# Kernel optimization log

Measured on AMD Instinct MI355X. Metric: run time of the kernel, lower is better.

The kernel has to match this reference:

```python
import jax, jax.numpy as jnp
import numpy as np

B, N, C, H = 2, 2048, 256, 8
HD = C // H
LN_EPS = 1e-5
BN_EPS = 1e-5  # eval-mode BatchNorm with running_mean=0, running_var=1


def _ln(x, g, b):
    # LayerNorm over last dim
    m = jnp.mean(x, axis=-1, keepdims=True)
    v = jnp.mean((x - m) ** 2, axis=-1, keepdims=True)
    return (x - m) * jax.lax.rsqrt(v + LN_EPS) * g + b


def _ln_cn(x, g, b):
    # x: [B,C,N], normalize over C (torch does transpose -> LN -> transpose)
    return jnp.swapaxes(_ln(jnp.swapaxes(x, 1, 2), g, b), 1, 2)


def _cdist(a, b):
    # a: [B,N,D], b: [B,M,D] -> [B,N,M] euclidean
    d2 = (jnp.sum(a * a, -1)[:, :, None] + jnp.sum(b * b, -1)[:, None, :]
          - 2.0 * jnp.einsum('bnd,bmd->bnm', a, b))
    return jnp.sqrt(jnp.maximum(d2, 0.0))


def _conv1x1(w, x, b=None):
    # w: [O,C], x: [B,C,N]
    y = jnp.einsum('oc,bcn->bon', w, x)
    return y if b is None else y + b[None, :, None]


def setup_inputs() -> dict:
    key = jax.random.key(0)
    ks = jax.random.split(key, 32)
    s = 0.02
    inp = {
        'xyz_A': jax.random.normal(ks[0], (B, N, 3), jnp.float32),
        'featA': jax.random.normal(ks[1], (B, C, N), jnp.float32),
        'xyz_B': jax.random.normal(ks[2], (B, N, 3), jnp.float32),
        'featB': jax.random.normal(ks[3], (B, C, N), jnp.float32),
        'ln_in_g': jnp.ones((C,), jnp.float32),
        'ln_in_b': jnp.zeros((C,), jnp.float32),
        'Wq': jax.random.normal(ks[4], (C, C), jnp.float32) * s,
        'bq': jnp.zeros((C,), jnp.float32),
        'Wk': jax.random.normal(ks[5], (C, C), jnp.float32) * s,
        'bk': jnp.zeros((C,), jnp.float32),
        'Wv': jax.random.normal(ks[6], (C, C), jnp.float32) * s,
        'bv': jnp.zeros((C,), jnp.float32),
        'sb_w1': jax.random.normal(ks[7], (H // 2, 1), jnp.float32) * s,
        'sb_bn_g': jnp.ones((H // 2,), jnp.float32),
        'sb_bn_b': jnp.zeros((H // 2,), jnp.float32),
        'sb_w2': jax.random.normal(ks[8], (H, H // 2), jnp.float32) * s,
        'sb_b2': jnp.zeros((H,), jnp.float32),
        'Wqd': jax.random.normal(ks[9], (C, C), jnp.float32) * s,
        'bqd': jnp.zeros((C,), jnp.float32),
        'Wkd': jax.random.normal(ks[10], (C, C), jnp.float32) * s,
        'bkd': jnp.zeros((C,), jnp.float32),
        'ln_sim_g': jnp.ones((C,), jnp.float32),
        'ln_sim_b': jnp.zeros((C,), jnp.float32),
        'ln_dis_g': jnp.ones((C,), jnp.float32),
        'ln_dis_b': jnp.zeros((C,), jnp.float32),
        'Wf1': jax.random.normal(ks[11], (2 * C, 3 * C), jnp.float32) * s,
        'bnf_g': jnp.ones((2 * C,), jnp.float32),
        'bnf_b': jnp.zeros((2 * C,), jnp.float32),
        'Wf2': jax.random.normal(ks[12], (C, 2 * C), jnp.float32) * s,
        'bf2': jnp.zeros((C,), jnp.float32),
    }
    return inp


def reference(xyz_A, featA, xyz_B, featB, ln_in_g, ln_in_b, Wq, bq, Wk, bk, Wv, bv,
              sb_w1, sb_bn_g, sb_bn_b, sb_w2, sb_b2, Wqd, bqd, Wkd, bkd,
              ln_sim_g, ln_sim_b, ln_dis_g, ln_dis_b, Wf1, bnf_g, bnf_b, Wf2, bf2):
    featA_norm = _ln_cn(featA, ln_in_g, ln_in_b)  # [B,C,N]

    # spatial bias: cdist -> 1x1 conv2d MLP over channel dim
    dist = _cdist(xyz_A, xyz_B)  # [B,N,N]
    h = jnp.einsum('oi,binm->bonm', sb_w1, -dist[:, None])  # [B,H/2,N,N]
    h = h * (sb_bn_g / np.sqrt(1.0 + BN_EPS))[None, :, None, None] + sb_bn_b[None, :, None, None]
    h = jax.nn.relu(h)
    spatial_bias = jnp.einsum('oi,binm->bonm', sb_w2, h) + sb_b2[None, :, None, None]  # [B,H,N,N]

    # similarity path
    q = _conv1x1(Wq, featA_norm, bq).reshape(B, H, HD, N).transpose(0, 1, 3, 2)  # [B,H,N,hd]
    k = _conv1x1(Wk, featB, bk).reshape(B, H, HD, N).transpose(0, 1, 3, 2)
    sim_scores = jnp.einsum('bhnd,bhmd->bhnm', q, k) / np.sqrt(HD) + spatial_bias

    # dissimilarity path: feature-space cdist
    qd = jnp.swapaxes(_conv1x1(Wqd, featA_norm, bqd), 1, 2)  # [B,N,C]
    kd = jnp.swapaxes(_conv1x1(Wkd, featB, bkd), 1, 2)
    dissim_scores = _cdist(qd, kd)[:, None] + spatial_bias  # [B,H,N,N]

    sim_w = jax.nn.softmax(sim_scores, axis=-1)
    dis_w = jax.nn.softmax(dissim_scores, axis=-1)

    v = _conv1x1(Wv, featB, bv).reshape(B, H, HD, N).transpose(0, 1, 3, 2)  # [B,H,N,hd]
    ctx_sim = jnp.einsum('bhnm,bhmd->bhnd', sim_w, v).transpose(0, 1, 3, 2).reshape(B, C, N)
    ctx_sim = _ln_cn(ctx_sim, ln_sim_g, ln_sim_b)
    ctx_dis = jnp.einsum('bhnm,bhmd->bhnd', dis_w, v).transpose(0, 1, 3, 2).reshape(B, C, N)
    ctx_dis = _ln_cn(ctx_dis, ln_dis_g, ln_dis_b)

    fused_in = jnp.concatenate([featA_norm, ctx_sim, ctx_dis], axis=1)  # [B,3C,N]
    f = jnp.einsum('oc,bcn->bon', Wf1, fused_in)
    f = f * (bnf_g / np.sqrt(1.0 + BN_EPS))[None, :, None] + bnf_b[None, :, None]
    f = jax.nn.relu(f)
    fused = jnp.einsum('oc,bcn->bon', Wf2, f) + bf2[None, :, None]

    return fused + featA  # residual (in_channel == out_channel -> Identity)
```

## Files before the change

kernel.cpp:

```cpp
#include <hip/hip_runtime.h>
#include <math.h>

#define B_ 2
#define N_ 2048
#define C_ 256
#define H_ 8
#define HD_ 32
constexpr float LN_EPS_ = 1e-5f;
constexpr float BN_EPS_ = 1e-5f;
constexpr float LOG2E_ = 1.4426950408889634f;
constexpr float ISDL_ = 0.17677669529663687f * 1.4426950408889634f;

typedef __attribute__((ext_vector_type(8))) short bf16x8;
typedef __attribute__((ext_vector_type(4))) float f32x4;

static __device__ inline ushort f2bf(float x) {
    union { float f; uint u; } c{x};
    uint r = (c.u + 0x7FFF + ((c.u >> 16) & 1)) >> 16;
    return (ushort)r;
}
static __device__ inline float bf2f(ushort u) {
    union { uint i; float f; } c; c.i = ((uint)u) << 16; return c.f;
}
static __device__ inline float lane_bcast(float v, int srclane) {
    return __int_as_float(__builtin_amdgcn_ds_bpermute(srclane * 4, __float_as_int(v)));
}
static __device__ inline uint pack_bf2(float lo, float hi) {
    uint ul = __float_as_uint(lo) + 0x8000u;
    uint uh = __float_as_uint(hi) + 0x8000u;
    return __builtin_amdgcn_perm(uh, ul, 0x07060302u);
}

__global__ __launch_bounds__(256)
void k_wconv(const float* __restrict__ Wq, const float* __restrict__ Wqd,
             const float* __restrict__ Wk, const float* __restrict__ Wkd,
             const float* __restrict__ Wv, const float* __restrict__ Wf1,
             const float* __restrict__ Wf2, ushort* __restrict__ dst)
{
    size_t e0 = ((size_t)blockIdx.x * 256 + threadIdx.x) * 8;
    const float* src = Wq; size_t base = 0;
    if (e0 >= 65536)  { src = Wqd; base = 65536; }
    if (e0 >= 131072) { src = Wk;  base = 131072; }
    if (e0 >= 196608) { src = Wkd; base = 196608; }
    if (e0 >= 262144) { src = Wv;  base = 262144; }
    if (e0 >= 327680) { src = Wf1; base = 327680; }
    if (e0 >= 720896) { src = Wf2; base = 720896; }
    float4 a = *(const float4*)(src + (e0 - base));
    float4 b = *(const float4*)(src + (e0 - base) + 4);
    ushort o[8] = {f2bf(a.x), f2bf(a.y), f2bf(a.z), f2bf(a.w),
                   f2bf(b.x), f2bf(b.y), f2bf(b.z), f2bf(b.w)};
    *(uint4*)(dst + e0) = *(uint4*)o;
}

__global__ __launch_bounds__(512)
void k_bconcat(const float* __restrict__ bq, const float* __restrict__ bqd,
               const float* __restrict__ bk, const float* __restrict__ bkd,
               float* __restrict__ bqqd, float* __restrict__ bkkd)
{
    int t = threadIdx.x;
    bqqd[t] = (t < 256) ? bq[t] : bqd[t - 256];
    bkkd[t] = (t < 256) ? bk[t] : bkd[t - 256];
}

template<bool DO_LN>
__global__ __launch_bounds__(256)
void k_ln_transpose(const float* __restrict__ x,
                    const float* __restrict__ g,
                    const float* __restrict__ bt,
                    ushort* __restrict__ out, int ld)
{
    __shared__ float tile[C_][65];
    __shared__ float red_s[4][64];
    __shared__ float red_q[4][64];
    __shared__ float ms[64];
    __shared__ float rs[64];

    const int b  = blockIdx.x / (N_ / 64);
    const int n0 = (blockIdx.x % (N_ / 64)) * 64;
    const int tid = threadIdx.x;

    for (int i = 0; i < 64; ++i) {
        int c = i * 4 + (tid >> 6);
        int n = tid & 63;
        tile[c][n] = x[((size_t)b * C_ + c) * N_ + n0 + n];
    }
    __syncthreads();

    float gv = 0.f, bv = 0.f;
    if (DO_LN) { gv = g[tid]; bv = bt[tid]; }

    if (DO_LN) {
        const int nl = tid & 63, part = tid >> 6;
        float s = 0.f, q = 0.f;
        for (int j = 0; j < 64; ++j) {
            float v = tile[part * 64 + j][nl];
            s += v; q += v * v;
        }
        red_s[part][nl] = s; red_q[part][nl] = q;
        __syncthreads();
        if (tid < 64) {
            float ss = red_s[0][tid] + red_s[1][tid] + red_s[2][tid] + red_s[3][tid];
            float qq = red_q[0][tid] + red_q[1][tid] + red_q[2][tid] + red_q[3][tid];
            float mean = ss * (1.0f / C_);
            float var  = qq * (1.0f / C_) - mean * mean;
            ms[tid] = mean;
            rs[tid] = rsqrtf(var + LN_EPS_);
        }
        __syncthreads();
    }

    for (int i = 0; i < 64; ++i) {
        float v = tile[tid][i];
        if (DO_LN) v = (v - ms[i]) * rs[i] * gv + bv;
        out[((size_t)b * N_ + n0 + i) * ld + tid] = f2bf(v);
    }
}

template<int EPI, int OUT>
__global__ __launch_bounds__(256)
void k_gemm_bf(const ushort* __restrict__ A, int lda, size_t sAz,
               const ushort* __restrict__ Bw, int ldb, size_t sBz,
               void* __restrict__ Cout_, int ldc, size_t sCz,
               int K,
               const float* __restrict__ aux1,
               const float* __restrict__ aux2)
{
    const int z = blockIdx.z;
    A  += (size_t)z * sAz;
    Bw += (size_t)z * sBz;

    const int r0 = blockIdx.x * 64;
    const int c0 = blockIdx.y * 64;
    const int tid = threadIdx.x;
    const int w = tid >> 6, lane = tid & 63;
    const int wr = w >> 1, wc = w & 1;
    const int ql = lane & 15, g = lane >> 4;

    __shared__ ushort As[64][40];
    __shared__ ushort Bs[64][40];

    f32x4 acc[2][2] = {};
    const int srow = tid >> 2;
    const int sk   = (tid & 3) * 8;

    for (int k0 = 0; k0 < K; k0 += 32) {
        bf16x8 av = *(const bf16x8*)&A[(size_t)(r0 + srow) * lda + k0 + sk];
        bf16x8 bv = *(const bf16x8*)&Bw[(size_t)(c0 + srow) * ldb + k0 + sk];
        __syncthreads();
        *(bf16x8*)&As[srow][sk] = av;
        *(bf16x8*)&Bs[srow][sk] = bv;
        __syncthreads();
        bf16x8 af[2], bf[2];
        #pragma unroll
        for (int i = 0; i < 2; ++i) {
            af[i] = *(const bf16x8*)&As[wr * 32 + i * 16 + ql][8 * g];
            bf[i] = *(const bf16x8*)&Bs[wc * 32 + i * 16 + ql][8 * g];
        }
        #pragma unroll
        for (int mi = 0; mi < 2; ++mi)
            #pragma unroll
            for (int ni = 0; ni < 2; ++ni)
                acc[mi][ni] = __builtin_amdgcn_mfma_f32_16x16x32_bf16(af[mi], bf[ni], acc[mi][ni], 0, 0, 0);
    }

    const float inv_bn = rsqrtf(1.0f + BN_EPS_);
    float*  Cf = (float*)Cout_  + (size_t)z * sCz;
    ushort* Cb = (ushort*)Cout_ + (size_t)z * sCz;
    #pragma unroll
    for (int mi = 0; mi < 2; ++mi) {
        #pragma unroll
        for (int ni = 0; ni < 2; ++ni) {
            #pragma unroll
            for (int r = 0; r < 4; ++r) {
                int row = r0 + wr * 32 + mi * 16 + 4 * g + r;
                int col = c0 + wc * 32 + ni * 16 + ql;
                float v = acc[mi][ni][r];
                if (EPI == 0) {
                    v += aux1[col];
                } else if (EPI == 1) {
                    float qnv = aux1[(size_t)z * N_ + row];
                    float knv = aux2[(size_t)z * N_ + col];
                    v = sqrtf(fmaxf(qnv + knv - 2.0f * v, 0.f)) * LOG2E_;
                } else if (EPI == 2) {
                    v = fmaxf(v * (aux1[col] * inv_bn) + aux2[col], 0.f);
                } else if (EPI == 3) {
                    v += aux1[row];
                }
                if (OUT == 0) Cf[(size_t)row * ldc + col] = v;
                else          Cb[(size_t)row * ldc + col] = f2bf(v);
            }
        }
    }
}

__global__ __launch_bounds__(256)
void k_rownorm(const ushort* __restrict__ x, int ld, float* __restrict__ outn)
{
    const int r = blockIdx.x * 4 + (threadIdx.x >> 6);
    const int lane = threadIdx.x & 63;
    uint2 pv = *(const uint2*)&x[(size_t)r * ld + lane * 4];
    float v0 = bf2f((ushort)(pv.x & 0xffff)), v1 = bf2f((ushort)(pv.x >> 16));
    float v2 = bf2f((ushort)(pv.y & 0xffff)), v3 = bf2f((ushort)(pv.y >> 16));
    float s = v0 * v0 + v1 * v1 + v2 * v2 + v3 * v3;
    #pragma unroll
    for (int off = 32; off; off >>= 1) s += __shfl_xor(s, off);
    if (lane == 0) outn[r] = s;
}

#define QLD_ 512
__global__ __launch_bounds__(512, 4)
void k_attn6(const ushort* __restrict__ q_bf,
             const ushort* __restrict__ k_bf,
             const ushort* __restrict__ v_c,
             const float* __restrict__ xyzA,
             const float* __restrict__ xyzB,
             const ushort* __restrict__ cdb,
             const float* __restrict__ sb_w1, const float* __restrict__ sb_bn_g,
             const float* __restrict__ sb_bn_b, const float* __restrict__ sb_w2,
             const float* __restrict__ sb_b2,
             ushort* __restrict__ pc,
             float* __restrict__ pml)
{
    __shared__ float  biasL[4][16][66];
    __shared__ float  cds[16][68];
    __shared__ ushort ps[8][16][72];
    __shared__ float  w2Ls[4][4];
    __shared__ float  b2Ls[4];

    const int n0 = blockIdx.x * 16;
    const int b  = blockIdx.y;
    const int hg   = blockIdx.z & 1;
    const int half = blockIdx.z >> 1;
    const size_t bN = (size_t)b * N_;
    const int tid = threadIdx.x;
    const int w = tid >> 6, lane = tid & 63;
    const int path = w >> 2, hl = w & 3;
    const int h = hg * 4 + hl;
    const int ql = lane & 15, g = lane >> 4;

    if (tid < 4) {
        b2Ls[tid] = sb_b2[hg * 4 + tid] * LOG2E_;
        #pragma unroll
        for (int i = 0; i < 4; ++i) w2Ls[tid][i] = sb_w2[(hg * 4 + tid) * 4 + i] * LOG2E_;
    }

    const float inv_bn = rsqrtf(1.0f + BN_EPS_);
    float w1s_[4], bnb_[4];
    #pragma unroll
    for (int i = 0; i < 4; ++i) {
        w1s_[i] = sb_w1[i] * sb_bn_g[i] * inv_bn;
        bnb_[i] = sb_bn_b[i];
    }

    const int cq = tid >> 5, cm2 = tid & 31;
    const float ax = xyzA[(bN + n0 + cq) * 3 + 0];
    const float ay = xyzA[(bN + n0 + cq) * 3 + 1];
    const float az = xyzA[(bN + n0 + cq) * 3 + 2];

    bf16x8 qfrag = {};
    if (path == 0)
        qfrag = *(const bf16x8*)&q_bf[(bN + n0 + ql) * QLD_ + h * 32 + 8 * g];

    float m_i = -INFINITY, l_i = 0.f;
    f32x4 ctx0 = {0.f, 0.f, 0.f, 0.f};
    f32x4 ctx1 = {0.f, 0.f, 0.f, 0.f};
    const f32x4 zf = {0.f, 0.f, 0.f, 0.f};

    const int tBeg = half * (N_ / 128);
    const int tEnd = tBeg + (N_ / 128);

    for (int t = tBeg; t < tEnd; ++t) {
        const int m0 = t * 64;
        __syncthreads();

        {
            const int mA = m0 + 2 * cm2;
            const float* pb = xyzB + (bN + mA) * 3;
            float bx0 = pb[0], by0 = pb[1], bz0 = pb[2];
            float bx1 = pb[3], by1 = pb[4], bz1 = pb[5];
            float dx0 = ax - bx0, dy0 = ay - by0, dz0 = az - bz0;
            float dx1 = ax - bx1, dy1 = ay - by1, dz1 = az - bz1;
            float d0 = sqrtf(dx0 * dx0 + dy0 * dy0 + dz0 * dz0);
            float d1 = sqrtf(dx1 * dx1 + dy1 * dy1 + dz1 * dz1);
            float f0[4], f1[4];
            #pragma unroll
            for (int i = 0; i < 4; ++i) {
                f0[i] = fmaxf(fmaf(-w1s_[i], d0, bnb_[i]), 0.f);
                f1[i] = fmaxf(fmaf(-w1s_[i], d1, bnb_[i]), 0.f);
            }
            #pragma unroll
            for (int hh = 0; hh < 4; ++hh) {
                const f32x4 w2v = *(const f32x4*)w2Ls[hh];
                float b0 = b2Ls[hh], b1 = b2Ls[hh];
                #pragma unroll
                for (int i = 0; i < 4; ++i) {
                    b0 = fmaf(w2v[i], f0[i], b0);
                    b1 = fmaf(w2v[i], f1[i], b1);
                }
                *(float2*)&biasL[hh][cq][2 * cm2] = make_float2(b0, b1);
            }
            uint cv = *(const uint*)&cdb[(bN + n0 + cq) * (size_t)N_ + mA];
            cds[cq][2 * cm2]     = __uint_as_float(cv << 16);
            cds[cq][2 * cm2 + 1] = __uint_as_float(cv & 0xffff0000u);
        }
        __syncthreads();

        bf16x8 af[4];
        if (path == 0) {
            #pragma unroll
            for (int mt = 0; mt < 4; ++mt)
                af[mt] = *(const bf16x8*)&k_bf[(bN + m0 + mt * 16 + ql) * QLD_ + h * 32 + 8 * g];
        }
        bf16x8 vb[2][2];
        #pragma unroll
        for (int kb = 0; kb < 2; ++kb)
            #pragma unroll
            for (int dt = 0; dt < 2; ++dt)
                vb[kb][dt] = *(const bf16x8*)&v_c[((size_t)b * C_ + h * 32 + dt * 16 + ql) * N_ + m0 + kb * 32 + 8 * g];

        float s[16];
        #pragma unroll
        for (int mt = 0; mt < 4; ++mt) {
            float2 blo = *(const float2*)&biasL[hl][ql][16 * mt + 4 * g];
            float2 bhi = *(const float2*)&biasL[hl][ql][16 * mt + 4 * g + 2];
            s[4 * mt + 0] = blo.x;
            s[4 * mt + 1] = blo.y;
            s[4 * mt + 2] = bhi.x;
            s[4 * mt + 3] = bhi.y;
        }

        if (path == 0) {
            #pragma unroll
            for (int mt = 0; mt < 4; ++mt) {
                f32x4 sf = __builtin_amdgcn_mfma_f32_16x16x32_bf16(af[mt], qfrag, zf, 0, 0, 0);
                #pragma unroll
                for (int r = 0; r < 4; ++r)
                    s[4 * mt + r] = fmaf(sf[r], ISDL_, s[4 * mt + r]);
            }
        } else {
            #pragma unroll
            for (int mt = 0; mt < 4; ++mt) {
                f32x4 cv = *(const f32x4*)&cds[ql][16 * mt + 4 * g];
                #pragma unroll
                for (int r = 0; r < 4; ++r)
                    s[4 * mt + r] += cv[r];
            }
        }

        float t0 = fmaxf(s[0], s[1]),   t1 = fmaxf(s[2], s[3]);
        float t2 = fmaxf(s[4], s[5]),   t3 = fmaxf(s[6], s[7]);
        float t4 = fmaxf(s[8], s[9]),   t5 = fmaxf(s[10], s[11]);
        float t6 = fmaxf(s[12], s[13]), t7 = fmaxf(s[14], s[15]);
        t0 = fmaxf(t0, t1); t2 = fmaxf(t2, t3);
        t4 = fmaxf(t4, t5); t6 = fmaxf(t6, t7);
        float tmax = fmaxf(fmaxf(t0, t2), fmaxf(t4, t6));
        tmax = fmaxf(tmax, __shfl_xor(tmax, 16));
        tmax = fmaxf(tmax, __shfl_xor(tmax, 32));
        if (!__all(tmax <= m_i + 8.0f)) {
            float mnew = fmaxf(m_i, tmax);
            float scl = exp2f(m_i - mnew);
            l_i *= scl;
            #pragma unroll
            for (int r = 0; r < 4; ++r) {
                float sr = lane_bcast(scl, 4 * g + r);
                ctx0[r] *= sr; ctx1[r] *= sr;
            }
            m_i = mnew;
        }
        float lsum = 0.f;
        #pragma unroll
        for (int j = 0; j < 16; ++j) {
            float pj = exp2f(s[j] - m_i);
            s[j] = pj;
            lsum += pj;
        }
        lsum += __shfl_xor(lsum, 16);
        lsum += __shfl_xor(lsum, 32);
        l_i += lsum;

        #pragma unroll
        for (int mt = 0; mt < 4; ++mt) {
            uint2 pk;
            pk.x = pack_bf2(s[4 * mt + 0], s[4 * mt + 1]);
            pk.y = pack_bf2(s[4 * mt + 2], s[4 * mt + 3]);
            *(uint2*)&ps[w][ql][16 * mt + 4 * g] = pk;
        }

        #pragma unroll
        for (int kb = 0; kb < 2; ++kb) {
            bf16x8 pa = *(const bf16x8*)&ps[w][ql][kb * 32 + 8 * g];
            ctx0 = __builtin_amdgcn_mfma_f32_16x16x32_bf16(pa, vb[kb][0], ctx0, 0, 0, 0);
            ctx1 = __builtin_amdgcn_mfma_f32_16x16x32_bf16(pa, vb[kb][1], ctx1, 0, 0, 0);
        }
    }

    const size_t sl = (size_t)(half * 2 + path) * (B_ * N_);
    #pragma unroll
    for (int r = 0; r < 4; ++r) {
        size_t base = (sl + bN + n0 + 4 * g + r) * C_ + h * 32;
        pc[base + ql]      = f2bf(ctx0[r]);
        pc[base + 16 + ql] = f2bf(ctx1[r]);
    }
    if (g == 0) {
        size_t mlb = ((sl + bN + n0 + ql) * H_ + h) * 2;
        pml[mlb]     = m_i;
        pml[mlb + 1] = l_i;
    }
}

__global__ __launch_bounds__(256)
void k_merge_ln(const ushort* __restrict__ pc, const float* __restrict__ pml,
                const float* __restrict__ g_sim, const float* __restrict__ b_sim,
                const float* __restrict__ g_dis, const float* __restrict__ b_dis,
                ushort* __restrict__ fused_bf)
{
    __shared__ float rs_[4], rq_[4];
    const int row = blockIdx.x;
    const int path = blockIdx.y;
    const int c = threadIdx.x;
    const int h = c >> 5;
    const size_t i0 = (size_t)(0 * 2 + path) * (B_ * N_) + row;
    const size_t i1 = (size_t)(1 * 2 + path) * (B_ * N_) + row;
    const float m0 = pml[(i0 * H_ + h) * 2], l0 = pml[(i0 * H_ + h) * 2 + 1];
    const float m1 = pml[(i1 * H_ + h) * 2], l1 = pml[(i1 * H_ + h) * 2 + 1];
    const float M = fmaxf(m0, m1);
    const float w0 = exp2f(m0 - M), w1 = exp2f(m1 - M);
    const float il = 1.0f / fmaf(l0, w0, l1 * w1);
    const float v = fmaf(bf2f(pc[i0 * C_ + c]), w0, bf2f(pc[i1 * C_ + c]) * w1) * il;

    float s = v, q = v * v;
    #pragma unroll
    for (int off = 32; off; off >>= 1) { s += __shfl_xor(s, off); q += __shfl_xor(q, off); }
    const int wv = c >> 6, lane = c & 63;
    if (lane == 0) { rs_[wv] = s; rq_[wv] = q; }
    __syncthreads();
    float ss = rs_[0] + rs_[1] + rs_[2] + rs_[3];
    float qq = rq_[0] + rq_[1] + rq_[2] + rq_[3];
    float mean = ss * (1.0f / C_);
    float var  = qq * (1.0f / C_) - mean * mean;
    float rstd = rsqrtf(var + LN_EPS_);
    const float* gp = path ? g_dis : g_sim;
    const float* bp = path ? b_dis : b_sim;
    fused_bf[(size_t)row * (3 * C_) + C_ + path * C_ + c] =
        f2bf((v - mean) * rstd * gp[c] + bp[c]);
}

__global__ __launch_bounds__(256)
void k_transpose_add(const float* __restrict__ fused_t,
                     const float* __restrict__ featA,
                     float* __restrict__ out)
{
    __shared__ float t[64][65];
    const int n0 = blockIdx.x * 64, c0 = blockIdx.y * 64, b = blockIdx.z;
    const int tid = threadIdx.x;
    #pragma unroll
    for (int i = 0; i < 16; ++i) {
        int e = i * 256 + tid;
        int nn = e >> 6, cc = e & 63;
        t[nn][cc] = fused_t[((size_t)b * N_ + n0 + nn) * C_ + c0 + cc];
    }
    __syncthreads();
    #pragma unroll
    for (int i = 0; i < 16; ++i) {
        int e = i * 256 + tid;
        int cc = e >> 6, nn = e & 63;
        size_t idx = ((size_t)b * C_ + c0 + cc) * N_ + n0 + nn;
        out[idx] = t[nn][cc] + featA[idx];
    }
}

extern "C" void kernel_launch(void* const* d_in, const int* in_sizes, int n_in,
                              void* d_out, int out_size, void* d_ws, size_t ws_size,
                              hipStream_t stream)
{
    const float* xyz_A   = (const float*)d_in[0];
    const float* featA   = (const float*)d_in[1];
    const float* xyz_B   = (const float*)d_in[2];
    const float* featB   = (const float*)d_in[3];
    const float* ln_in_g = (const float*)d_in[4];
    const float* ln_in_b = (const float*)d_in[5];
    const float* Wq  = (const float*)d_in[6];
    const float* bq  = (const float*)d_in[7];
    const float* Wk  = (const float*)d_in[8];
    const float* bk  = (const float*)d_in[9];
    const float* Wv  = (const float*)d_in[10];
    const float* bv  = (const float*)d_in[11];
    const float* sb_w1   = (const float*)d_in[12];
    const float* sb_bn_g = (const float*)d_in[13];
    const float* sb_bn_b = (const float*)d_in[14];
    const float* sb_w2   = (const float*)d_in[15];
    const float* sb_b2   = (const float*)d_in[16];
    const float* Wqd = (const float*)d_in[17];
    const float* bqd = (const float*)d_in[18];
    const float* Wkd = (const float*)d_in[19];
    const float* bkd = (const float*)d_in[20];
    const float* ln_sim_g = (const float*)d_in[21];
    const float* ln_sim_b = (const float*)d_in[22];
    const float* ln_dis_g = (const float*)d_in[23];
    const float* ln_dis_b = (const float*)d_in[24];
    const float* Wf1   = (const float*)d_in[25];
    const float* bnf_g = (const float*)d_in[26];
    const float* bnf_b = (const float*)d_in[27];
    const float* Wf2   = (const float*)d_in[28];
    const float* bf2   = (const float*)d_in[29];
    float* out = (float*)d_out;

    float* ws = (float*)d_ws;
    size_t off = 0;
    auto alloc = [&](size_t n) { float* p = ws + off; off += n; return p; };
    const size_t RN = (size_t)B_ * N_;

    ushort* fused_bf = (ushort*)alloc(RN * 384);
    ushort* featB_bf = (ushort*)alloc(RN * 128);
    ushort* qqd_bf   = (ushort*)alloc(RN * 256);
    ushort* kkd_bf   = (ushort*)alloc(RN * 256);
    ushort* v_bf     = (ushort*)alloc(RN * 128);
    ushort* wbf      = (ushort*)alloc(425984);
    float*  bqqd     = alloc(512);
    float*  bkkd     = alloc(512);
    float*  qn       = alloc(RN);
    float*  kn       = alloc(RN);
    ushort* cd_bf    = (ushort*)alloc((size_t)B_ * N_ * N_ / 2);
    ushort* pc       = (ushort*)alloc(4 * RN * C_ / 2);
    float*  pml      = alloc(4 * RN * H_ * 2);

    ushort* q_bf  = qqd_bf;
    ushort* qd_bf = qqd_bf + 256;
    ushort* k_bf  = kkd_bf;
    ushort* kd_bf = kkd_bf + 256;
    ushort* fh      = cd_bf;
    float*  fused_t = (float*)(cd_bf + (size_t)RN * 512);

    ushort* wqqd_bf = wbf;
    ushort* wkkd_bf = wbf + 131072;
    ushort* wv_bf   = wbf + 262144;
    ushort* wf1_bf  = wbf + 327680;
    ushort* wf2_bf  = wbf + 720896;
    (void)ws_size; (void)in_sizes; (void)n_in; (void)out_size;

    dim3 blk(256);

    k_wconv<<<dim3(416), blk, 0, stream>>>(Wq, Wqd, Wk, Wkd, Wv, Wf1, Wf2, wbf);
    k_bconcat<<<dim3(1), dim3(512), 0, stream>>>(bq, bqd, bk, bkd, bqqd, bkkd);
    k_ln_transpose<true ><<<dim3(B_ * (N_ / 64)), blk, 0, stream>>>(featA, ln_in_g, ln_in_b, fused_bf, 3 * C_);
    k_ln_transpose<false><<<dim3(B_ * (N_ / 64)), blk, 0, stream>>>(featB, nullptr, nullptr, featB_bf, C_);

    k_gemm_bf<0,1><<<dim3(RN / 64, 8, 1), blk, 0, stream>>>(fused_bf, 3 * C_, 0, wqqd_bf, C_, 0, qqd_bf, 512, 0, C_, bqqd, nullptr);
    k_gemm_bf<0,1><<<dim3(RN / 64, 8, 1), blk, 0, stream>>>(featB_bf, C_,     0, wkkd_bf, C_, 0, kkd_bf, 512, 0, C_, bkkd, nullptr);
    k_gemm_bf<3,1><<<dim3(C_ / 64, N_ / 64, B_), blk, 0, stream>>>(wv_bf, C_, 0, featB_bf, C_, (size_t)N_ * C_, v_bf, N_, (size_t)C_ * N_, C_, bv, nullptr);

    k_rownorm<<<dim3(RN / 4), blk, 0, stream>>>(qd_bf, 512, qn);
    k_rownorm<<<dim3(RN / 4), blk, 0, stream>>>(kd_bf, 512, kn);
    k_gemm_bf<1,1><<<dim3(N_ / 64, N_ / 64, B_), blk, 0, stream>>>(qd_bf, 512, (size_t)N_ * 512,
                                                                   kd_bf, 512, (size_t)N_ * 512,
                                                                   cd_bf, N_, (size_t)N_ * N_, C_, qn, kn);

    k_attn6<<<dim3(N_ / 16, B_, 4), dim3(512), 0, stream>>>(q_bf, k_bf, v_bf, xyz_A, xyz_B, cd_bf,
                                                            sb_w1, sb_bn_g, sb_bn_b, sb_w2, sb_b2,
                                                            pc, pml);
    k_merge_ln<<<dim3(RN, 2), blk, 0, stream>>>(pc, pml, ln_sim_g, ln_sim_b, ln_dis_g, ln_dis_b, fused_bf);

    k_gemm_bf<2,1><<<dim3(RN / 64, 8, 1), blk, 0, stream>>>(fused_bf, 3 * C_, 0, wf1_bf, 3 * C_, 0, fh, 2 * C_, 0, 3 * C_, bnf_g, bnf_b);
    k_gemm_bf<0,0><<<dim3(RN / 64, 4, 1), blk, 0, stream>>>(fh, 2 * C_, 0, wf2_bf, 2 * C_, 0, fused_t, C_, 0, 2 * C_, bf2, nullptr);

    k_transpose_add<<<dim3(N_ / 64, C_ / 64, B_), blk, 0, stream>>>(fused_t, featA, out);
}
```

Baseline: 207.5 us.

## Double-buffer attention bias/cdist tiles in LDS with register prefetch

```diff
diff --git a/kernel.cpp b/kernel.cpp
--- a/kernel.cpp
+++ b/kernel.cpp
@@ -22,6 +22,8 @@
 static __device__ inline float bf2f(ushort u) {
     union { uint i; float f; } c; c.i = ((uint)u) << 16; return c.f;
 }
+static __device__ inline float bf_lo(uint u) { return __uint_as_float(u << 16); }
+static __device__ inline float bf_hi(uint u) { return __uint_as_float(u & 0xffff0000u); }
 static __device__ inline float lane_bcast(float v, int srclane) {
     return __int_as_float(__builtin_amdgcn_ds_bpermute(srclane * 4, __float_as_int(v)));
 }
@@ -209,7 +211,7 @@
 
 #define QLD_ 512
 __global__ __launch_bounds__(512, 4)
-void k_attn6(const ushort* __restrict__ q_bf,
+void k_attn7(const ushort* __restrict__ q_bf,
              const ushort* __restrict__ k_bf,
              const ushort* __restrict__ v_c,
              const float* __restrict__ xyzA,
@@ -221,8 +223,8 @@
              ushort* __restrict__ pc,
              float* __restrict__ pml)
 {
-    __shared__ float  biasL[4][16][66];
-    __shared__ float  cds[16][68];
+    __shared__ ushort biasL[2][4][16][72];
+    __shared__ ushort cdsL[2][16][72];
     __shared__ ushort ps[8][16][72];
     __shared__ float  w2Ls[4][4];
     __shared__ float  b2Ls[4];
@@ -269,42 +271,54 @@
     const int tBeg = half * (N_ / 128);
     const int tEnd = tBeg + (N_ / 128);
 
+    float xb[6]; uint cdv;
+    auto coop_load = [&](int t) {
+        const int mA = t * 64 + 2 * cm2;
+        const float* pb = xyzB + (bN + mA) * 3;
+        #pragma unroll
+        for (int i = 0; i < 6; ++i) xb[i] = pb[i];
+        cdv = *(const uint*)&cdb[(bN + n0 + cq) * (size_t)N_ + mA];
+    };
+    auto coop_write = [&](int buf) {
+        float dx0 = ax - xb[0], dy0 = ay - xb[1], dz0 = az - xb[2];
+        float dx1 = ax - xb[3], dy1 = ay - xb[4], dz1 = az - xb[5];
+        float d0 = sqrtf(dx0 * dx0 + dy0 * dy0 + dz0 * dz0);
+        float d1 = sqrtf(dx1 * dx1 + dy1 * dy1 + dz1 * dz1);
+        float f0[4], f1[4];
+        #pragma unroll
+        for (int i = 0; i < 4; ++i) {
+            f0[i] = fmaxf(fmaf(-w1s_[i], d0, bnb_[i]), 0.f);
+            f1[i] = fmaxf(fmaf(-w1s_[i], d1, bnb_[i]), 0.f);
+        }
+        #pragma unroll
+        for (int hh = 0; hh < 4; ++hh) {
+            const f32x4 w2v = *(const f32x4*)w2Ls[hh];
+            float b0 = b2Ls[hh], b1 = b2Ls[hh];
+            #pragma unroll
+            for (int i = 0; i < 4; ++i) {
+                b0 = fmaf(w2v[i], f0[i], b0);
+                b1 = fmaf(w2v[i], f1[i], b1);
+            }
+            *(uint*)&biasL[buf][hh][cq][2 * cm2] = pack_bf2(b0, b1);
+        }
+        *(uint*)&cdsL[buf][cq][2 * cm2] = cdv;
+    };
+
+    __syncthreads();
+    coop_load(tBeg);
+    coop_write(0);
+    if (tBeg + 1 < tEnd) coop_load(tBeg + 1);
+    __syncthreads();
+
     for (int t = tBeg; t < tEnd; ++t) {
+        const int cur = (t - tBeg) & 1;
+
+        if (t + 1 < tEnd) {
+            coop_write(cur ^ 1);
+            if (t + 2 < tEnd) coop_load(t + 2);
+        }
+
         const int m0 = t * 64;
-        __syncthreads();
-
-        {
-            const int mA = m0 + 2 * cm2;
-            const float* pb = xyzB + (bN + mA) * 3;
-            float bx0 = pb[0], by0 = pb[1], bz0 = pb[2];
-            float bx1 = pb[3], by1 = pb[4], bz1 = pb[5];
-            float dx0 = ax - bx0, dy0 = ay - by0, dz0 = az - bz0;
-            float dx1 = ax - bx1, dy1 = ay - by1, dz1 = az - bz1;
-            float d0 = sqrtf(dx0 * dx0 + dy0 * dy0 + dz0 * dz0);
-            float d1 = sqrtf(dx1 * dx1 + dy1 * dy1 + dz1 * dz1);
-            float f0[4], f1[4];
-            #pragma unroll
-            for (int i = 0; i < 4; ++i) {
-                f0[i] = fmaxf(fmaf(-w1s_[i], d0, bnb_[i]), 0.f);
-                f1[i] = fmaxf(fmaf(-w1s_[i], d1, bnb_[i]), 0.f);
-            }
-            #pragma unroll
-            for (int hh = 0; hh < 4; ++hh) {
-                const f32x4 w2v = *(const f32x4*)w2Ls[hh];
-                float b0 = b2Ls[hh], b1 = b2Ls[hh];
-                #pragma unroll
-                for (int i = 0; i < 4; ++i) {
-                    b0 = fmaf(w2v[i], f0[i], b0);
-                    b1 = fmaf(w2v[i], f1[i], b1);
-                }
-                *(float2*)&biasL[hh][cq][2 * cm2] = make_float2(b0, b1);
-            }
-            uint cv = *(const uint*)&cdb[(bN + n0 + cq) * (size_t)N_ + mA];
-            cds[cq][2 * cm2]     = __uint_as_float(cv << 16);
-            cds[cq][2 * cm2 + 1] = __uint_as_float(cv & 0xffff0000u);
-        }
-        __syncthreads();
-
         bf16x8 af[4];
         if (path == 0) {
             #pragma unroll
@@ -321,15 +335,15 @@
         float s[16];
         #pragma unroll
         for (int mt = 0; mt < 4; ++mt) {
-            float2 blo = *(const float2*)&biasL[hl][ql][16 * mt + 4 * g];
-            float2 bhi = *(const float2*)&biasL[hl][ql][16 * mt + 4 * g + 2];
-            s[4 * mt + 0] = blo.x;
-            s[4 * mt + 1] = blo.y;
-            s[4 * mt + 2] = bhi.x;
-            s[4 * mt + 3] = bhi.y;
+            uint2 bw = *(const uint2*)&biasL[cur][hl][ql][16 * mt + 4 * g];
+            s[4 * mt + 0] = bf_lo(bw.x);
+            s[4 * mt + 1] = bf_hi(bw.x);
+            s[4 * mt + 2] = bf_lo(bw.y);
+            s[4 * mt + 3] = bf_hi(bw.y);
         }
 
         if (path == 0) {
+            __builtin_amdgcn_s_setprio(1);
             #pragma unroll
             for (int mt = 0; mt < 4; ++mt) {
                 f32x4 sf = __builtin_amdgcn_mfma_f32_16x16x32_bf16(af[mt], qfrag, zf, 0, 0, 0);
@@ -337,13 +351,15 @@
                 for (int r = 0; r < 4; ++r)
                     s[4 * mt + r] = fmaf(sf[r], ISDL_, s[4 * mt + r]);
             }
+            __builtin_amdgcn_s_setprio(0);
         } else {
             #pragma unroll
             for (int mt = 0; mt < 4; ++mt) {
-                f32x4 cv = *(const f32x4*)&cds[ql][16 * mt + 4 * g];
-                #pragma unroll
-                for (int r = 0; r < 4; ++r)
-                    s[4 * mt + r] += cv[r];
+                uint2 cw = *(const uint2*)&cdsL[cur][ql][16 * mt + 4 * g];
+                s[4 * mt + 0] += bf_lo(cw.x);
+                s[4 * mt + 1] += bf_hi(cw.x);
+                s[4 * mt + 2] += bf_lo(cw.y);
+                s[4 * mt + 3] += bf_hi(cw.y);
             }
         }
 
@@ -386,12 +402,16 @@
             *(uint2*)&ps[w][ql][16 * mt + 4 * g] = pk;
         }
 
+        __builtin_amdgcn_s_setprio(1);
         #pragma unroll
         for (int kb = 0; kb < 2; ++kb) {
             bf16x8 pa = *(const bf16x8*)&ps[w][ql][kb * 32 + 8 * g];
             ctx0 = __builtin_amdgcn_mfma_f32_16x16x32_bf16(pa, vb[kb][0], ctx0, 0, 0, 0);
             ctx1 = __builtin_amdgcn_mfma_f32_16x16x32_bf16(pa, vb[kb][1], ctx1, 0, 0, 0);
         }
+        __builtin_amdgcn_s_setprio(0);
+
+        __syncthreads();
     }
 
     const size_t sl = (size_t)(half * 2 + path) * (B_ * N_);
@@ -555,7 +575,7 @@
                                                                    kd_bf, 512, (size_t)N_ * 512,
                                                                    cd_bf, N_, (size_t)N_ * N_, C_, qn, kn);
 
-    k_attn6<<<dim3(N_ / 16, B_, 4), dim3(512), 0, stream>>>(q_bf, k_bf, v_bf, xyz_A, xyz_B, cd_bf,
+    k_attn7<<<dim3(N_ / 16, B_, 4), dim3(512), 0, stream>>>(q_bf, k_bf, v_bf, xyz_A, xyz_B, cd_bf,
                                                             sb_w1, sb_bn_g, sb_bn_b, sb_w2, sb_b2,
                                                             pc, pml);
     k_merge_ln<<<dim3(RN, 2), blk, 0, stream>>>(pc, pml, ln_sim_g, ln_sim_b, ln_dis_g, ln_dis_b, fused_bf);
```

New measurement: 204.8 us (median of 2 runs). No clear change (-1.3%).
